# Kernel optimization log

Hardware: AMD Instinct MI355X
Metric: run time of the kernel (lower is better)

The kernel has to match this reference:

```python
import jax, jax.numpy as jnp
import numpy as np

D = 2048
H = 16
HD = 128
INNER = H * HD
EPS = 1e-6


def rmsnorm(x, w):
    var = jnp.mean(x * x, axis=-1, keepdims=True)
    return x * jax.lax.rsqrt(var + EPS) * w


def setup_inputs() -> dict:
    key = jax.random.key(0)
    ks = jax.random.split(key, 10)
    B, T, N_ws, T_corr = 2, 2048, 64, 512
    scale = 1.0 / np.sqrt(D)
    return {
        "hidden_states": jax.random.normal(ks[0], (B, T, D), jnp.float32),
        "workspace": jax.random.normal(ks[1], (B, N_ws, D), jnp.float32),
        "correction_tokens": jax.random.normal(ks[2], (B, T_corr, D), jnp.float32),
        "correction_mask": jax.random.randint(ks[3], (B, T_corr), 0, 2, jnp.int32),
        "ln_q_w": jnp.ones((D,), jnp.float32),
        "ln_kv_w": jnp.ones((D,), jnp.float32),
        "Wq": jax.random.normal(ks[4], (D, INNER), jnp.float32) * scale,
        "Wk": jax.random.normal(ks[5], (D, INNER), jnp.float32) * scale,
        "Wv": jax.random.normal(ks[6], (D, INNER), jnp.float32) * scale,
        "Wo": jax.random.normal(ks[7], (INNER, D), jnp.float32) * scale,
    }


def reference(hidden_states, workspace, correction_tokens, correction_mask,
              ln_q_w, ln_kv_w, Wq, Wk, Wv, Wo):
    B, T, _ = hidden_states.shape
    N_ws = workspace.shape[1]
    # kv context = [workspace ; correction_tokens]
    kv_context = jnp.concatenate([workspace, correction_tokens], axis=1)  # (B, N_kv, D)
    N_kv = kv_context.shape[1]
    ws_mask = jnp.ones((B, N_ws), hidden_states.dtype)
    kv_mask = jnp.concatenate([ws_mask, correction_mask.astype(hidden_states.dtype)], axis=1)  # (B, N_kv)

    h = rmsnorm(hidden_states, ln_q_w)
    kv = rmsnorm(kv_context, ln_kv_w)

    q = (h @ Wq).reshape(B, T, H, HD)        # (B,T,H,hd)
    k = (kv @ Wk).reshape(B, N_kv, H, HD)
    v = (kv @ Wv).reshape(B, N_kv, H, HD)

    scores = jnp.einsum("bthd,bshd->bhts", q, k) / np.sqrt(HD)  # (B,H,T,N_kv)
    mask = (kv_mask != 0)[:, None, None, :]                      # (B,1,1,N_kv)
    scores = jnp.where(mask, scores, -jnp.inf)
    attn = jax.nn.softmax(scores, axis=-1)
    attn = jnp.nan_to_num(attn, nan=0.0)
    # dropout is identity in eval mode
    out = jnp.einsum("bhts,bshd->bthd", attn, v).reshape(B, T, INNER)
    return out @ Wo
```

## Files before the change

### kernel.cpp

```cpp
#include <hip/hip_runtime.h>
#include <hip/hip_bf16.h>
#include <math.h>

typedef __bf16 bf16;
typedef __attribute__((ext_vector_type(8))) __bf16 bf16x8;
typedef __attribute__((ext_vector_type(4))) __bf16 bf16x4;
typedef __attribute__((ext_vector_type(4))) float f32x4;

#define D_DIM 2048
#define NKV   576

__device__ inline void gld_lds16(const void* g, void* l) {
    void* gg = const_cast<void*>(g);
    __builtin_amdgcn_global_load_lds(
        (__attribute__((address_space(1))) void*)gg,
        (__attribute__((address_space(3))) void*)l, 16, 0, 0);
}

#define PH_BARRIER() do { __builtin_amdgcn_s_barrier(); asm volatile("" ::: "memory"); } while (0)
#define VMCNT(n)     asm volatile("s_waitcnt vmcnt(" #n ")" ::: "memory")

__global__ __launch_bounds__(256) void prep(
    const float* __restrict__ hidden, const float* __restrict__ wsp,
    const float* __restrict__ corr, const float* __restrict__ lnq,
    const float* __restrict__ lnkv,
    const float* __restrict__ Wq, const float* __restrict__ Wk,
    const float* __restrict__ Wv, const float* __restrict__ Wo,
    bf16* __restrict__ hb, bf16* __restrict__ kvb,
    bf16* __restrict__ WqT, bf16* __restrict__ WkvT, bf16* __restrict__ WoT)
{
    __shared__ float tile[32][33];
    __shared__ float p[4];
    const int id = blockIdx.x, t = threadIdx.x;

    if (id < 16384) {
        const int wz = id >> 12, wy = (id >> 6) & 63, wx = id & 63;
        const float* in; bf16* out;
        switch (wz) {
            case 0:  in = Wq; out = WqT; break;
            case 1:  in = Wk; out = WkvT; break;
            case 2:  in = Wv; out = WkvT + 2048ull * 2048; break;
            default: in = Wo; out = WoT; break;
        }
        const int r0 = wy * 32, c0 = wx * 32;
        const int r = t >> 3, c = (t & 7) * 4;
        float4 v = *(const float4*)(in + (long)(r0 + r) * 2048 + c0 + c);
        tile[r][c] = v.x; tile[r][c + 1] = v.y;
        tile[r][c + 2] = v.z; tile[r][c + 3] = v.w;
        __syncthreads();
        bf16x4 o = { (bf16)tile[c][r], (bf16)tile[c + 1][r],
                     (bf16)tile[c + 2][r], (bf16)tile[c + 3][r] };
        *(bf16x4*)(out + (long)(c0 + r) * 2048 + r0 + c) = o;
        return;
    }

    const int rr0 = id - 16384;
    const float* xr; const float* w; bf16* yr;
    if (rr0 < 4096) {
        xr = hidden + (long)rr0 * D_DIM; w = lnq; yr = hb + (long)rr0 * D_DIM;
    } else if (rr0 < 4224) {
        const int rr = rr0 - 4096;
        xr = wsp + (long)rr * D_DIM; w = lnkv;
        yr = kvb + ((long)(rr >> 6) * NKV + (rr & 63)) * D_DIM;
    } else {
        const int rr = rr0 - 4224;
        xr = corr + (long)rr * D_DIM; w = lnkv;
        yr = kvb + ((long)(rr >> 9) * NKV + 64 + (rr & 511)) * D_DIM;
    }

    float4 v0 = *(const float4*)(xr + t * 4);
    float4 v1 = *(const float4*)(xr + 1024 + t * 4);
    float ss = v0.x * v0.x + v0.y * v0.y + v0.z * v0.z + v0.w * v0.w
             + v1.x * v1.x + v1.y * v1.y + v1.z * v1.z + v1.w * v1.w;
#pragma unroll
    for (int off = 32; off; off >>= 1) ss += __shfl_xor(ss, off);
    if ((t & 63) == 0) p[t >> 6] = ss;
    __syncthreads();
    const float rs = rsqrtf((p[0] + p[1] + p[2] + p[3]) * (1.0f / 2048.0f) + 1e-6f);

    float4 w0 = *(const float4*)(w + t * 4);
    float4 w1 = *(const float4*)(w + 1024 + t * 4);
    bf16x4 o0 = { (bf16)(v0.x * rs * w0.x), (bf16)(v0.y * rs * w0.y),
                  (bf16)(v0.z * rs * w0.z), (bf16)(v0.w * rs * w0.w) };
    bf16x4 o1 = { (bf16)(v1.x * rs * w1.x), (bf16)(v1.y * rs * w1.y),
                  (bf16)(v1.z * rs * w1.z), (bf16)(v1.w * rs * w1.w) };
    *(bf16x4*)(yr + t * 4) = o0;
    *(bf16x4*)(yr + 1024 + t * 4) = o1;
}

__global__ __launch_bounds__(512, 2) void proj_all(
    const bf16* __restrict__ hb, const bf16* __restrict__ kvb,
    const bf16* __restrict__ WqT, const bf16* __restrict__ WkvT,
    bf16* __restrict__ qb, bf16* __restrict__ kb, bf16* __restrict__ vtb)
{
    __shared__ __align__(16) bf16 smem[4][16384];
    bf16* const EA = smem[0]; bf16* const EB = smem[1];
    bf16* const OA = smem[2]; bf16* const OB = smem[3];

    const int id0 = blockIdx.x;
    const int id = (id0 & 7) * 26 + (id0 >> 3);
    const bf16 *A, *B; int m0, n0; bool isQ;
    if (id < 128) {
        isQ = true;  A = hb;  B = WqT;
        m0 = (id >> 3) * 256; n0 = (id & 7) * 256;
    } else {
        const int kd = id - 128;
        isQ = false; A = kvb; B = WkvT;
        m0 = (kd >> 4) * 256; n0 = (kd & 15) * 256;
    }

    const int tid = threadIdx.x, lane = tid & 63, w = tid >> 6;
    const int wm = (w >> 2) * 128, wn = (w & 3) * 64;
    const int fr = lane & 15, fg = lane >> 4;

    f32x4 acc[8][4] = {};
    bf16x8 af[4][2], bg[4][2];

    auto stage = [&](const bf16* base, int row0, int k, bf16* dst) {
#pragma unroll
        for (int q = 0; q < 2; ++q) {
            const int c = q * 512 + tid;
            const int r = c >> 3, cl = (c & 7) ^ (r & 7);
            gld_lds16(base + (long)(row0 + r) * 2048 + k + cl * 8, dst + c * 8);
        }
    };
    auto load_af = [&](const bf16* t, int ib) {
#pragma unroll
        for (int i = 0; i < 4; ++i)
#pragma unroll
            for (int s = 0; s < 2; ++s) {
                const int row = wm + (ib + i) * 16 + fr;
                af[i][s] = *(const bf16x8*)(t + ((row << 3) + ((s * 4 + fg) ^ (fr & 7))) * 8);
            }
    };
    auto load_bg = [&](const bf16* t, int jb) {
#pragma unroll
        for (int j = 0; j < 2; ++j)
#pragma unroll
            for (int s = 0; s < 2; ++s) {
                const int row = wn + (jb + j) * 16 + fr;
                bg[jb + j][s] = *(const bf16x8*)(t + ((row << 3) + ((s * 4 + fg) ^ (fr & 7))) * 8);
            }
    };
    auto mfma16 = [&](int ib, int jb) {
        __builtin_amdgcn_s_setprio(1);
#pragma unroll
        for (int s = 0; s < 2; ++s)
#pragma unroll
            for (int i = 0; i < 4; ++i)
#pragma unroll
                for (int j = 0; j < 2; ++j)
                    acc[ib + i][jb + j] = __builtin_amdgcn_mfma_f32_16x16x32_bf16(
                        af[i][s], bg[jb + j][s], acc[ib + i][jb + j], 0, 0, 0);
        __builtin_amdgcn_s_setprio(0);
    };

    stage(A, m0,        0, EA); stage(A, m0 + 128,  0, EA + 8192);
    stage(B, n0,        0, EB); stage(B, n0 + 128,  0, EB + 8192);
    stage(B, n0,       64, OB); stage(B, n0 + 128, 64, OB + 8192);
    VMCNT(4);
    PH_BARRIER();

    for (int it = 0; it < 16; ++it) {
        const int kO  = (it * 128 +  64) & 2047;
        const int kE2 = (it * 128 + 128) & 2047;
        const int kO2 = (it * 128 + 192) & 2047;
        load_af(EA, 0); load_bg(EB, 0);
        stage(A, m0, kO, OA);
        PH_BARRIER(); mfma16(0, 0); PH_BARRIER();
        load_bg(EB, 2);
        stage(A, m0 + 128, kO, OA + 8192);
        PH_BARRIER(); mfma16(0, 2); PH_BARRIER();
        load_af(EA, 4);
        stage(B, n0, kE2, EB);
        PH_BARRIER(); mfma16(4, 2); PH_BARRIER();
        stage(B, n0 + 128, kE2, EB + 8192);
        PH_BARRIER(); mfma16(4, 0); VMCNT(4); PH_BARRIER();
        load_af(OA, 0); load_bg(OB, 0);
        stage(A, m0, kE2, EA);
        PH_BARRIER(); mfma16(0, 0); PH_BARRIER();
        load_bg(OB, 2);
        stage(A, m0 + 128, kE2, EA + 8192);
        PH_BARRIER(); mfma16(0, 2); PH_BARRIER();
        load_af(OA, 4);
        stage(B, n0, kO2, OB);
        PH_BARRIER(); mfma16(4, 2); PH_BARRIER();
        stage(B, n0 + 128, kO2, OB + 8192);
        PH_BARRIER(); mfma16(4, 0); VMCNT(4); PH_BARRIER();
    }

    VMCNT(0);
    __syncthreads();

    const int er = fg * 4;
    if (isQ || n0 < 2048) {
        bf16* C = isQ ? qb : kb;
        const int mlim = isQ ? 4096 : 1152;
#pragma unroll
        for (int i = 0; i < 8; ++i)
#pragma unroll
            for (int j = 0; j < 4; ++j) {
                const int n = n0 + wn + j * 16 + fr;
#pragma unroll
                for (int r = 0; r < 4; ++r) {
                    const int m = m0 + wm + i * 16 + er + r;
                    if (m < mlim)
                        C[(long)m * 2048 + n] = (bf16)acc[i][j][r];
                }
            }
        return;
    }

    bf16* T = &smem[0][0];
#pragma unroll
    for (int p = 0; p < 2; ++p) {
        if (p) __syncthreads();
        if ((wn >> 7) == p) {
            const int nb = wn - p * 128;
#pragma unroll
            for (int i = 0; i < 8; ++i)
#pragma unroll
                for (int j = 0; j < 4; ++j) {
                    const int nl = nb + j * 16 + fr;
#pragma unroll
                    for (int r = 0; r < 4; ++r)
                        T[nl * 264 + wm + i * 16 + er + r] = (bf16)acc[i][j][r];
                }
        }
        __syncthreads();
        const int hh = (n0 - 2048 + p * 128) >> 7;
        for (int e = tid; e < 128 * 64; e += 512) {
            const int d = e >> 6, mg = (e & 63) * 4;
            const int mm = m0 + mg;
            if (mm < 1152) {
                bf16x4 val = *(const bf16x4*)(T + d * 264 + mg);
                const int bb = mm >= NKV;
                const int s = mm - bb * NKV;
                *(bf16x4*)(vtb + ((long)((bb * 16 + hh) * 128 + d)) * NKV + s) = val;
            }
        }
    }
}

__global__ __launch_bounds__(512, 2) void gemm_final(
    const bf16* __restrict__ Ag, const bf16* __restrict__ Bg, float* __restrict__ C)
{
    __shared__ __align__(16) bf16 smem[49152];
    bf16* const EA = smem;           bf16* const EB = smem + 16384;
    bf16* const OA = smem + 24576;   bf16* const OB = smem + 40960;

    const int id0 = blockIdx.x;
    const int id = (id0 & 7) * 32 + (id0 >> 3);
    const int m0 = (id >> 4) * 256, n0 = (id & 15) * 128;

    const int tid = threadIdx.x, lane = tid & 63, w = tid >> 6;
    const int wm = (w >> 1) * 64, wn = (w & 1) * 64;
    const int fr = lane & 15, fg = lane >> 4;

    f32x4 acc[4][4] = {};
    bf16x8 af[2][2], bg[4][2];

    auto stage = [&](const bf16* base, int row0, int k, bf16* dst) {
#pragma unroll
        for (int q = 0; q < 2; ++q) {
            const int c = q * 512 + tid;
            const int r = c >> 3, cl = (c & 7) ^ (r & 7);
            gld_lds16(base + (long)(row0 + r) * 2048 + k + cl * 8, dst + c * 8);
        }
    };
    auto load_af = [&](const bf16* t, int ib) {
#pragma unroll
        for (int i = 0; i < 2; ++i)
#pragma unroll
            for (int s = 0; s < 2; ++s) {
                const int row = wm + (ib + i) * 16 + fr;
                af[i][s] = *(const bf16x8*)(t + ((row << 3) + ((s * 4 + fg) ^ (fr & 7))) * 8);
            }
    };
    auto load_bg = [&](const bf16* t, int jb) {
#pragma unroll
        for (int j = 0; j < 2; ++j)
#pragma unroll
            for (int s = 0; s < 2; ++s) {
                const int row = wn + (jb + j) * 16 + fr;
                bg[jb + j][s] = *(const bf16x8*)(t + ((row << 3) + ((s * 4 + fg) ^ (fr & 7))) * 8);
            }
    };
    auto mfma8 = [&](int ib, int jb) {
        __builtin_amdgcn_s_setprio(1);
#pragma unroll
        for (int s = 0; s < 2; ++s)
#pragma unroll
            for (int i = 0; i < 2; ++i)
#pragma unroll
                for (int j = 0; j < 2; ++j)
                    acc[ib + i][jb + j] = __builtin_amdgcn_mfma_f32_16x16x32_bf16(
                        af[i][s], bg[jb + j][s], acc[ib + i][jb + j], 0, 0, 0);
        __builtin_amdgcn_s_setprio(0);
    };

    stage(Ag, m0,       0, EA); stage(Ag, m0 + 128, 0, EA + 8192);
    stage(Bg, n0,       0, EB);
    stage(Bg, n0,      64, OB);
    VMCNT(2);
    PH_BARRIER();

    for (int it = 0; it < 16; ++it) {
        const int kO  = (it * 128 +  64) & 2047;
        const int kE2 = (it * 128 + 128) & 2047;
        const int kO2 = (it * 128 + 192) & 2047;
        load_af(EA, 0); load_bg(EB, 0);
        stage(Ag, m0, kO, OA);
        PH_BARRIER(); mfma8(0, 0); PH_BARRIER();
        load_bg(EB, 2);
        stage(Ag, m0 + 128, kO, OA + 8192);
        PH_BARRIER(); mfma8(0, 2); PH_BARRIER();
        load_af(EA, 2);
        stage(Bg, n0, kE2, EB);
        PH_BARRIER(); mfma8(2, 2); PH_BARRIER();
        stage(Ag, m0, kE2, EA);
        PH_BARRIER(); mfma8(2, 0); VMCNT(4); PH_BARRIER();
        load_af(OA, 0); load_bg(OB, 0);
        stage(Ag, m0 + 128, kE2, EA + 8192);
        PH_BARRIER(); mfma8(0, 0); PH_BARRIER();
        load_bg(OB, 2);
        PH_BARRIER(); mfma8(0, 2); PH_BARRIER();
        load_af(OA, 2);
        stage(Bg, n0, kO2, OB);
        PH_BARRIER(); mfma8(2, 2); PH_BARRIER();
        PH_BARRIER(); mfma8(2, 0); VMCNT(2); PH_BARRIER();
    }

    VMCNT(0);
    __syncthreads();

    const int er = fg * 4;
#pragma unroll
    for (int i = 0; i < 4; ++i)
#pragma unroll
        for (int j = 0; j < 4; ++j) {
            const int n = n0 + wn + j * 16 + fr;
#pragma unroll
            for (int r = 0; r < 4; ++r)
                C[(long)(m0 + wm + i * 16 + er + r) * 2048 + n] = acc[i][j][r];
        }
}

__global__ __launch_bounds__(256, 4) void flash_attn(
    const bf16* __restrict__ Q, const bf16* __restrict__ K,
    const bf16* __restrict__ VT, const int* __restrict__ cmask,
    bf16* __restrict__ O)
{
    __shared__ __align__(16) bf16 Ks[64 * 128];
    __shared__ __align__(16) bf16 VTs[128 * 64];

    const int qt = blockIdx.x, h = blockIdx.y, b = blockIdx.z;
    const int tid = threadIdx.x, lane = tid & 63, w = tid >> 6;
    const int fr = lane & 15, fg = lane >> 4;

    const bf16* qbase = Q + ((long)(b * 2048 + qt * 64)) * 2048 + h * 128;
    bf16x8 qf[4];
#pragma unroll
    for (int s = 0; s < 4; ++s)
        qf[s] = *(const bf16x8*)(qbase + (long)(w * 16 + fr) * 2048 + s * 32 + fg * 8);

    float m_r[4], l_r[4];
    f32x4 acc_o[8];
#pragma unroll
    for (int r = 0; r < 4; ++r) { m_r[r] = -3.0e38f; l_r[r] = 0.f; }
#pragma unroll
    for (int j = 0; j < 8; ++j) acc_o[j] = (f32x4){0.f, 0.f, 0.f, 0.f};

    const float scale2 = 0.12752792330124195f;
    const bf16* kbase = K + (long)b * NKV * 2048 + h * 128;
    const bf16* vbase = VT + ((long)(b * 16 + h)) * 128 * NKV;

    for (int kc = 0; kc < 9; ++kc) {
        const int kv0 = kc * 64;
#pragma unroll
        for (int p = 0; p < 4; ++p) {
            const int c = p * 256 + tid;
            const int r = c >> 4, cs = c & 15, cl = cs ^ (r & 15);
            gld_lds16(kbase + (long)(kv0 + r) * 2048 + cl * 8, Ks + c * 8);
        }
#pragma unroll
        for (int p = 0; p < 4; ++p) {
            const int c = p * 256 + tid;
            const int r = c >> 3, cs = c & 7, cl = cs ^ (r & 7);
            gld_lds16(vbase + (long)r * NKV + kv0 + cl * 8, VTs + c * 8);
        }
        __syncthreads();

        f32x4 acc_s[4] = {};
#pragma unroll
        for (int s = 0; s < 4; ++s) {
#pragma unroll
            for (int j = 0; j < 4; ++j) {
                bf16x8 bg = *(const bf16x8*)(Ks +
                    ((j * 16 + fr) * 16 + ((s * 4 + fg) ^ fr)) * 8);
                acc_s[j] = __builtin_amdgcn_mfma_f32_16x16x32_bf16(qf[s], bg, acc_s[j], 0, 0, 0);
            }
        }

        float bias[4];
#pragma unroll
        for (int j = 0; j < 4; ++j) {
            const int kv = kv0 + j * 16 + fr;
            const bool valid = (kv < 64) || (cmask[b * 512 + kv - 64] != 0);
            bias[j] = valid ? 0.f : -1e30f;
        }
        float s_f[4][4];
        float mc[4] = {-3.0e38f, -3.0e38f, -3.0e38f, -3.0e38f};
#pragma unroll
        for (int j = 0; j < 4; ++j)
#pragma unroll
            for (int r = 0; r < 4; ++r) {
                float v = fmaf(acc_s[j][r], scale2, bias[j]);
                s_f[j][r] = v; mc[r] = fmaxf(mc[r], v);
            }
#pragma unroll
        for (int r = 0; r < 4; ++r) {
            mc[r] = fmaxf(mc[r], __shfl_xor(mc[r], 1));
            mc[r] = fmaxf(mc[r], __shfl_xor(mc[r], 2));
            mc[r] = fmaxf(mc[r], __shfl_xor(mc[r], 4));
            mc[r] = fmaxf(mc[r], __shfl_xor(mc[r], 8));
        }
        float alpha[4];
#pragma unroll
        for (int r = 0; r < 4; ++r) {
            const float mn = fmaxf(m_r[r], mc[r]);
            alpha[r] = __builtin_amdgcn_exp2f(m_r[r] - mn);
            m_r[r] = mn;
        }
        float rs[4] = {0.f, 0.f, 0.f, 0.f};
#pragma unroll
        for (int j = 0; j < 4; ++j)
#pragma unroll
            for (int r = 0; r < 4; ++r) {
                const float pv = __builtin_amdgcn_exp2f(s_f[j][r] - m_r[r]);
                s_f[j][r] = pv; rs[r] += pv;
            }
#pragma unroll
        for (int r = 0; r < 4; ++r) {
            rs[r] += __shfl_xor(rs[r], 1);
            rs[r] += __shfl_xor(rs[r], 2);
            rs[r] += __shfl_xor(rs[r], 4);
            rs[r] += __shfl_xor(rs[r], 8);
            l_r[r] = l_r[r] * alpha[r] + rs[r];
        }
#pragma unroll
        for (int j = 0; j < 8; ++j)
#pragma unroll
            for (int r = 0; r < 4; ++r) acc_o[j][r] *= alpha[r];

        __syncthreads();

        bf16* Ps = Ks;
#pragma unroll
        for (int j = 0; j < 4; ++j)
#pragma unroll
            for (int r = 0; r < 4; ++r)
                Ps[(w * 16 + fg * 4 + r) * 72 + j * 16 + fr] = (bf16)s_f[j][r];

#pragma unroll
        for (int s2 = 0; s2 < 2; ++s2) {
            bf16x8 af = *(const bf16x8*)(Ps + (w * 16 + fr) * 72 + s2 * 32 + fg * 8);
#pragma unroll
            for (int jd = 0; jd < 8; ++jd) {
                bf16x8 bg = *(const bf16x8*)(VTs +
                    ((jd * 16 + fr) * 8 + ((s2 * 4 + fg) ^ (fr & 7))) * 8);
                acc_o[jd] = __builtin_amdgcn_mfma_f32_16x16x32_bf16(af, bg, acc_o[jd], 0, 0, 0);
            }
        }
        __syncthreads();
    }

    bf16* obase = O + ((long)(b * 2048 + qt * 64)) * 2048 + h * 128;
#pragma unroll
    for (int r = 0; r < 4; ++r) {
        const float inv = 1.0f / l_r[r];
        const int row = w * 16 + fg * 4 + r;
#pragma unroll
        for (int jd = 0; jd < 8; ++jd)
            obase[(long)row * 2048 + jd * 16 + fr] = (bf16)(acc_o[jd][r] * inv);
    }
}

extern "C" void kernel_launch(void* const* d_in, const int* in_sizes, int n_in,
                              void* d_out, int out_size, void* d_ws, size_t ws_size,
                              hipStream_t stream)
{
    const float* hidden = (const float*)d_in[0];
    const float* wsp    = (const float*)d_in[1];
    const float* corr   = (const float*)d_in[2];
    const int*   cmask  = (const int*)d_in[3];
    const float* lnq    = (const float*)d_in[4];
    const float* lnkv   = (const float*)d_in[5];
    const float* Wq     = (const float*)d_in[6];
    const float* Wk     = (const float*)d_in[7];
    const float* Wv     = (const float*)d_in[8];
    const float* Wo     = (const float*)d_in[9];
    float* out = (float*)d_out;

    char* ws = (char*)d_ws;
    size_t off = 0;
    auto alloc = [&](size_t sz) { void* p = ws + off; off += (sz + 255) & ~(size_t)255; return p; };

    bf16* WqT   = (bf16*)alloc(2048ull * 2048 * 2);
    bf16* WkvT  = (bf16*)alloc(4096ull * 2048 * 2);
    bf16* WoT   = (bf16*)alloc(2048ull * 2048 * 2);
    bf16* hb    = (bf16*)alloc(4096ull * 2048 * 2);
    bf16* kvb   = (bf16*)alloc(1280ull * 2048 * 2);
    bf16* qb    = (bf16*)alloc(4096ull * 2048 * 2);
    bf16* kb    = (bf16*)alloc(1152ull * 2048 * 2);
    bf16* vtb   = (bf16*)alloc(4096ull * NKV * 2);
    bf16* aob   = (bf16*)alloc(4096ull * 2048 * 2);

    prep<<<21632, 256, 0, stream>>>(hidden, wsp, corr, lnq, lnkv,
                                    Wq, Wk, Wv, Wo, hb, kvb, WqT, WkvT, WoT);
    proj_all<<<208, 512, 0, stream>>>(hb, kvb, WqT, WkvT, qb, kb, vtb);
    flash_attn<<<dim3(32, 16, 2), 256, 0, stream>>>(qb, kb, vtb, cmask, aob);
    gemm_final<<<256, 512, 0, stream>>>(aob, WoT, out);
}
```

Measured before the change: 297.7 us.

## Enlarge weight-transpose tiles, precompute GEMM staging addresses, peel last K iteration

```diff
diff --git a/kernel.cpp b/kernel.cpp
--- a/kernel.cpp
+++ b/kernel.cpp
@@ -29,12 +29,13 @@
     bf16* __restrict__ hb, bf16* __restrict__ kvb,
     bf16* __restrict__ WqT, bf16* __restrict__ WkvT, bf16* __restrict__ WoT)
 {
-    __shared__ float tile[32][33];
+    __shared__ float tl[64][65];
     __shared__ float p[4];
     const int id = blockIdx.x, t = threadIdx.x;
 
-    if (id < 16384) {
-        const int wz = id >> 12, wy = (id >> 6) & 63, wx = id & 63;
+    if (id < 4096) {
+        const int wz = id >> 10, idx = id & 1023;
+        const int wy = idx >> 5, wx = idx & 31;
         const float* in; bf16* out;
         switch (wz) {
             case 0:  in = Wq; out = WqT; break;
@@ -42,19 +43,27 @@
             case 2:  in = Wv; out = WkvT + 2048ull * 2048; break;
             default: in = Wo; out = WoT; break;
         }
-        const int r0 = wy * 32, c0 = wx * 32;
-        const int r = t >> 3, c = (t & 7) * 4;
-        float4 v = *(const float4*)(in + (long)(r0 + r) * 2048 + c0 + c);
-        tile[r][c] = v.x; tile[r][c + 1] = v.y;
-        tile[r][c + 2] = v.z; tile[r][c + 3] = v.w;
+        const int r0 = wy * 64, c0 = wx * 64;
+        const int tr = t >> 4, tc = (t & 15) * 4;
+#pragma unroll
+        for (int q = 0; q < 4; ++q) {
+            const int r = tr + q * 16;
+            float4 v = *(const float4*)(in + (long)(r0 + r) * 2048 + c0 + tc);
+            tl[r][tc] = v.x; tl[r][tc + 1] = v.y;
+            tl[r][tc + 2] = v.z; tl[r][tc + 3] = v.w;
+        }
         __syncthreads();
-        bf16x4 o = { (bf16)tile[c][r], (bf16)tile[c + 1][r],
-                     (bf16)tile[c + 2][r], (bf16)tile[c + 3][r] };
-        *(bf16x4*)(out + (long)(c0 + r) * 2048 + r0 + c) = o;
+#pragma unroll
+        for (int q = 0; q < 4; ++q) {
+            const int orr = tr + q * 16;
+            bf16x4 o = { (bf16)tl[tc][orr], (bf16)tl[tc + 1][orr],
+                         (bf16)tl[tc + 2][orr], (bf16)tl[tc + 3][orr] };
+            *(bf16x4*)(out + (long)(c0 + orr) * 2048 + r0 + tc) = o;
+        }
         return;
     }
 
-    const int rr0 = id - 16384;
+    const int rr0 = id - 4096;
     const float* xr; const float* w; bf16* yr;
     if (rr0 < 4096) {
         xr = hidden + (long)rr0 * D_DIM; w = lnq; yr = hb + (long)rr0 * D_DIM;
@@ -116,31 +125,41 @@
     f32x4 acc[8][4] = {};
     bf16x8 af[4][2], bg[4][2];
 
-    auto stage = [&](const bf16* base, int row0, int k, bf16* dst) {
-#pragma unroll
-        for (int q = 0; q < 2; ++q) {
-            const int c = q * 512 + tid;
-            const int r = c >> 3, cl = (c & 7) ^ (r & 7);
-            gld_lds16(base + (long)(row0 + r) * 2048 + k + cl * 8, dst + c * 8);
-        }
-    };
-    auto load_af = [&](const bf16* t, int ib) {
+    const int aoff0 = (wm + fr) * 64 + (fg ^ (fr & 7)) * 8;
+    const int boff0 = (wn + fr) * 64 + (fg ^ (fr & 7)) * 8;
+    const int aoff1 = aoff0 ^ 32, boff1 = boff0 ^ 32;
+    const bf16* const pAE[2] = { EA + aoff0, EA + aoff1 };
+    const bf16* const pAO[2] = { OA + aoff0, OA + aoff1 };
+    const bf16* const pBE[2] = { EB + boff0, EB + boff1 };
+    const bf16* const pBO[2] = { OB + boff0, OB + boff1 };
+
+    const long toff = (long)(tid >> 3) * 2048 + (((tid & 7) ^ ((tid >> 3) & 7)) * 8);
+    const bf16* const gA0 = A + (long)m0 * 2048 + toff;
+    const bf16* const gA1 = gA0 + 262144;
+    const bf16* const gB0 = B + (long)n0 * 2048 + toff;
+    const bf16* const gB1 = gB0 + 262144;
+    bf16* const dT = (bf16*)smem + tid * 8;
+
+    auto stage2 = [&](const bf16* g, int k, int dslot) {
+        gld_lds16(g + k, dT + dslot);
+        gld_lds16(g + 131072 + k, dT + dslot + 4096);
+    };
+    enum { sEA0 = 0, sEA1 = 8192, sEB0 = 16384, sEB1 = 24576,
+           sOA0 = 32768, sOA1 = 40960, sOB0 = 49152, sOB1 = 57344 };
+
+    auto load_af = [&](const bf16* const p[2], int ib) {
 #pragma unroll
         for (int i = 0; i < 4; ++i)
 #pragma unroll
-            for (int s = 0; s < 2; ++s) {
-                const int row = wm + (ib + i) * 16 + fr;
-                af[i][s] = *(const bf16x8*)(t + ((row << 3) + ((s * 4 + fg) ^ (fr & 7))) * 8);
-            }
-    };
-    auto load_bg = [&](const bf16* t, int jb) {
+            for (int s = 0; s < 2; ++s)
+                af[i][s] = *(const bf16x8*)(p[s] + (ib + i) * 1024);
+    };
+    auto load_bg = [&](const bf16* const p[2], int jb) {
 #pragma unroll
         for (int j = 0; j < 2; ++j)
 #pragma unroll
-            for (int s = 0; s < 2; ++s) {
-                const int row = wn + (jb + j) * 16 + fr;
-                bg[jb + j][s] = *(const bf16x8*)(t + ((row << 3) + ((s * 4 + fg) ^ (fr & 7))) * 8);
-            }
+            for (int s = 0; s < 2; ++s)
+                bg[jb + j][s] = *(const bf16x8*)(p[s] + (jb + j) * 1024);
     };
     auto mfma16 = [&](int ib, int jb) {
         __builtin_amdgcn_s_setprio(1);
@@ -155,41 +174,56 @@
         __builtin_amdgcn_s_setprio(0);
     };
 
-    stage(A, m0,        0, EA); stage(A, m0 + 128,  0, EA + 8192);
-    stage(B, n0,        0, EB); stage(B, n0 + 128,  0, EB + 8192);
-    stage(B, n0,       64, OB); stage(B, n0 + 128, 64, OB + 8192);
+    stage2(gA0, 0, sEA0); stage2(gA1, 0, sEA1);
+    stage2(gB0, 0, sEB0); stage2(gB1, 0, sEB1);
+    stage2(gB0, 64, sOB0); stage2(gB1, 64, sOB1);
     VMCNT(4);
     PH_BARRIER();
 
-    for (int it = 0; it < 16; ++it) {
-        const int kO  = (it * 128 +  64) & 2047;
-        const int kE2 = (it * 128 + 128) & 2047;
-        const int kO2 = (it * 128 + 192) & 2047;
-        load_af(EA, 0); load_bg(EB, 0);
-        stage(A, m0, kO, OA);
+    for (int it = 0; it < 15; ++it) {
+        const int kO = it * 128 + 64, kE2 = it * 128 + 128, kO2 = it * 128 + 192;
+        load_af(pAE, 0); load_bg(pBE, 0);
+        stage2(gA0, kO, sOA0);
         PH_BARRIER(); mfma16(0, 0); PH_BARRIER();
-        load_bg(EB, 2);
-        stage(A, m0 + 128, kO, OA + 8192);
+        load_bg(pBE, 2);
+        stage2(gA1, kO, sOA1);
         PH_BARRIER(); mfma16(0, 2); PH_BARRIER();
-        load_af(EA, 4);
-        stage(B, n0, kE2, EB);
+        load_af(pAE, 4);
+        stage2(gB0, kE2, sEB0);
         PH_BARRIER(); mfma16(4, 2); PH_BARRIER();
-        stage(B, n0 + 128, kE2, EB + 8192);
+        stage2(gB1, kE2, sEB1);
         PH_BARRIER(); mfma16(4, 0); VMCNT(4); PH_BARRIER();
-        load_af(OA, 0); load_bg(OB, 0);
-        stage(A, m0, kE2, EA);
+        load_af(pAO, 0); load_bg(pBO, 0);
+        stage2(gA0, kE2, sEA0);
         PH_BARRIER(); mfma16(0, 0); PH_BARRIER();
-        load_bg(OB, 2);
-        stage(A, m0 + 128, kE2, EA + 8192);
+        load_bg(pBO, 2);
+        stage2(gA1, kE2, sEA1);
         PH_BARRIER(); mfma16(0, 2); PH_BARRIER();
-        load_af(OA, 4);
-        stage(B, n0, kO2, OB);
+        load_af(pAO, 4);
+        stage2(gB0, kO2, sOB0);
         PH_BARRIER(); mfma16(4, 2); PH_BARRIER();
-        stage(B, n0 + 128, kO2, OB + 8192);
+        stage2(gB1, kO2, sOB1);
         PH_BARRIER(); mfma16(4, 0); VMCNT(4); PH_BARRIER();
     }
-
-    VMCNT(0);
+    {
+        load_af(pAE, 0); load_bg(pBE, 0);
+        stage2(gA0, 1984, sOA0);
+        PH_BARRIER(); mfma16(0, 0); PH_BARRIER();
+        load_bg(pBE, 2);
+        stage2(gA1, 1984, sOA1);
+        PH_BARRIER(); mfma16(0, 2); PH_BARRIER();
+        load_af(pAE, 4);
+        PH_BARRIER(); mfma16(4, 2); PH_BARRIER();
+        PH_BARRIER(); mfma16(4, 0); VMCNT(0); PH_BARRIER();
+        load_af(pAO, 0); load_bg(pBO, 0);
+        PH_BARRIER(); mfma16(0, 0); PH_BARRIER();
+        load_bg(pBO, 2);
+        PH_BARRIER(); mfma16(0, 2); PH_BARRIER();
+        load_af(pAO, 4);
+        PH_BARRIER(); mfma16(4, 2); PH_BARRIER();
+        PH_BARRIER(); mfma16(4, 0); PH_BARRIER();
+    }
+
     __syncthreads();
 
     const int er = fg * 4;
@@ -213,10 +247,10 @@
 
     bf16* T = &smem[0][0];
 #pragma unroll
-    for (int p = 0; p < 2; ++p) {
-        if (p) __syncthreads();
-        if ((wn >> 7) == p) {
-            const int nb = wn - p * 128;
+    for (int p2 = 0; p2 < 2; ++p2) {
+        if (p2) __syncthreads();
+        if ((wn >> 7) == p2) {
+            const int nb = wn - p2 * 128;
 #pragma unroll
             for (int i = 0; i < 8; ++i)
 #pragma unroll
@@ -228,7 +262,7 @@
                 }
         }
         __syncthreads();
-        const int hh = (n0 - 2048 + p * 128) >> 7;
+        const int hh = (n0 - 2048 + p2 * 128) >> 7;
         for (int e = tid; e < 128 * 64; e += 512) {
             const int d = e >> 6, mg = (e & 63) * 4;
             const int mm = m0 + mg;
@@ -260,31 +294,40 @@
     f32x4 acc[4][4] = {};
     bf16x8 af[2][2], bg[4][2];
 
-    auto stage = [&](const bf16* base, int row0, int k, bf16* dst) {
-#pragma unroll
-        for (int q = 0; q < 2; ++q) {
-            const int c = q * 512 + tid;
-            const int r = c >> 3, cl = (c & 7) ^ (r & 7);
-            gld_lds16(base + (long)(row0 + r) * 2048 + k + cl * 8, dst + c * 8);
-        }
-    };
-    auto load_af = [&](const bf16* t, int ib) {
+    const int aoff0 = (wm + fr) * 64 + (fg ^ (fr & 7)) * 8;
+    const int boff0 = (wn + fr) * 64 + (fg ^ (fr & 7)) * 8;
+    const int aoff1 = aoff0 ^ 32, boff1 = boff0 ^ 32;
+    const bf16* const pAE[2] = { EA + aoff0, EA + aoff1 };
+    const bf16* const pAO[2] = { OA + aoff0, OA + aoff1 };
+    const bf16* const pBE[2] = { EB + boff0, EB + boff1 };
+    const bf16* const pBO[2] = { OB + boff0, OB + boff1 };
+
+    const long toff = (long)(tid >> 3) * 2048 + (((tid & 7) ^ ((tid >> 3) & 7)) * 8);
+    const bf16* const gA0 = Ag + (long)m0 * 2048 + toff;
+    const bf16* const gA1 = gA0 + 262144;
+    const bf16* const gB0 = Bg + (long)n0 * 2048 + toff;
+    bf16* const dT = smem + tid * 8;
+
+    auto stage2 = [&](const bf16* g, int k, int dslot) {
+        gld_lds16(g + k, dT + dslot);
+        gld_lds16(g + 131072 + k, dT + dslot + 4096);
+    };
+    enum { sEA0 = 0, sEA1 = 8192, sEB0 = 16384,
+           sOA0 = 24576, sOA1 = 32768, sOB0 = 40960 };
+
+    auto load_af = [&](const bf16* const p[2], int ib) {
 #pragma unroll
         for (int i = 0; i < 2; ++i)
 #pragma unroll
-            for (int s = 0; s < 2; ++s) {
-                const int row = wm + (ib + i) * 16 + fr;
-                af[i][s] = *(const bf16x8*)(t + ((row << 3) + ((s * 4 + fg) ^ (fr & 7))) * 8);
-            }
-    };
-    auto load_bg = [&](const bf16* t, int jb) {
+            for (int s = 0; s < 2; ++s)
+                af[i][s] = *(const bf16x8*)(p[s] + (ib + i) * 1024);
+    };
+    auto load_bg = [&](const bf16* const p[2], int jb) {
 #pragma unroll
         for (int j = 0; j < 2; ++j)
 #pragma unroll
-            for (int s = 0; s < 2; ++s) {
-                const int row = wn + (jb + j) * 16 + fr;
-                bg[jb + j][s] = *(const bf16x8*)(t + ((row << 3) + ((s * 4 + fg) ^ (fr & 7))) * 8);
-            }
+            for (int s = 0; s < 2; ++s)
+                bg[jb + j][s] = *(const bf16x8*)(p[s] + (jb + j) * 1024);
     };
     auto mfma8 = [&](int ib, int jb) {
         __builtin_amdgcn_s_setprio(1);
@@ -299,39 +342,54 @@
         __builtin_amdgcn_s_setprio(0);
     };
 
-    stage(Ag, m0,       0, EA); stage(Ag, m0 + 128, 0, EA + 8192);
-    stage(Bg, n0,       0, EB);
-    stage(Bg, n0,      64, OB);
+    stage2(gA0, 0, sEA0); stage2(gA1, 0, sEA1);
+    stage2(gB0, 0, sEB0);
+    stage2(gB0, 64, sOB0);
     VMCNT(2);
     PH_BARRIER();
 
-    for (int it = 0; it < 16; ++it) {
-        const int kO  = (it * 128 +  64) & 2047;
-        const int kE2 = (it * 128 + 128) & 2047;
-        const int kO2 = (it * 128 + 192) & 2047;
-        load_af(EA, 0); load_bg(EB, 0);
-        stage(Ag, m0, kO, OA);
+    for (int it = 0; it < 15; ++it) {
+        const int kO = it * 128 + 64, kE2 = it * 128 + 128, kO2 = it * 128 + 192;
+        load_af(pAE, 0); load_bg(pBE, 0);
+        stage2(gA0, kO, sOA0);
         PH_BARRIER(); mfma8(0, 0); PH_BARRIER();
-        load_bg(EB, 2);
-        stage(Ag, m0 + 128, kO, OA + 8192);
+        load_bg(pBE, 2);
+        stage2(gA1, kO, sOA1);
         PH_BARRIER(); mfma8(0, 2); PH_BARRIER();
-        load_af(EA, 2);
-        stage(Bg, n0, kE2, EB);
+        load_af(pAE, 2);
+        stage2(gB0, kE2, sEB0);
         PH_BARRIER(); mfma8(2, 2); PH_BARRIER();
-        stage(Ag, m0, kE2, EA);
+        stage2(gA0, kE2, sEA0);
         PH_BARRIER(); mfma8(2, 0); VMCNT(4); PH_BARRIER();
-        load_af(OA, 0); load_bg(OB, 0);
-        stage(Ag, m0 + 128, kE2, EA + 8192);
+        load_af(pAO, 0); load_bg(pBO, 0);
+        stage2(gA1, kE2, sEA1);
         PH_BARRIER(); mfma8(0, 0); PH_BARRIER();
-        load_bg(OB, 2);
+        load_bg(pBO, 2);
         PH_BARRIER(); mfma8(0, 2); PH_BARRIER();
-        load_af(OA, 2);
-        stage(Bg, n0, kO2, OB);
+        load_af(pAO, 2);
+        stage2(gB0, kO2, sOB0);
         PH_BARRIER(); mfma8(2, 2); PH_BARRIER();
         PH_BARRIER(); mfma8(2, 0); VMCNT(2); PH_BARRIER();
     }
-
-    VMCNT(0);
+    {
+        load_af(pAE, 0); load_bg(pBE, 0);
+        stage2(gA0, 1984, sOA0);
+        PH_BARRIER(); mfma8(0, 0); PH_BARRIER();
+        load_bg(pBE, 2);
+        stage2(gA1, 1984, sOA1);
+        PH_BARRIER(); mfma8(0, 2); PH_BARRIER();
+        load_af(pAE, 2);
+        PH_BARRIER(); mfma8(2, 2); PH_BARRIER();
+        PH_BARRIER(); mfma8(2, 0); VMCNT(0); PH_BARRIER();
+        load_af(pAO, 0); load_bg(pBO, 0);
+        PH_BARRIER(); mfma8(0, 0); PH_BARRIER();
+        load_bg(pBO, 2);
+        PH_BARRIER(); mfma8(0, 2); PH_BARRIER();
+        load_af(pAO, 2);
+        PH_BARRIER(); mfma8(2, 2); PH_BARRIER();
+        PH_BARRIER(); mfma8(2, 0); PH_BARRIER();
+    }
+
     __syncthreads();
 
     const int er = fg * 4;
@@ -396,9 +454,9 @@
         for (int s = 0; s < 4; ++s) {
 #pragma unroll
             for (int j = 0; j < 4; ++j) {
-                bf16x8 bg = *(const bf16x8*)(Ks +
+                bf16x8 bgv = *(const bf16x8*)(Ks +
                     ((j * 16 + fr) * 16 + ((s * 4 + fg) ^ fr)) * 8);
-                acc_s[j] = __builtin_amdgcn_mfma_f32_16x16x32_bf16(qf[s], bg, acc_s[j], 0, 0, 0);
+                acc_s[j] = __builtin_amdgcn_mfma_f32_16x16x32_bf16(qf[s], bgv, acc_s[j], 0, 0, 0);
             }
         }
 
@@ -464,12 +522,12 @@
 
 #pragma unroll
         for (int s2 = 0; s2 < 2; ++s2) {
-            bf16x8 af = *(const bf16x8*)(Ps + (w * 16 + fr) * 72 + s2 * 32 + fg * 8);
+            bf16x8 afv = *(const bf16x8*)(Ps + (w * 16 + fr) * 72 + s2 * 32 + fg * 8);
 #pragma unroll
             for (int jd = 0; jd < 8; ++jd) {
-                bf16x8 bg = *(const bf16x8*)(VTs +
+                bf16x8 bgv = *(const bf16x8*)(VTs +
                     ((jd * 16 + fr) * 8 + ((s2 * 4 + fg) ^ (fr & 7))) * 8);
-                acc_o[jd] = __builtin_amdgcn_mfma_f32_16x16x32_bf16(af, bg, acc_o[jd], 0, 0, 0);
+                acc_o[jd] = __builtin_amdgcn_mfma_f32_16x16x32_bf16(afv, bgv, acc_o[jd], 0, 0, 0);
             }
         }
         __syncthreads();
@@ -516,8 +574,8 @@
     bf16* vtb   = (bf16*)alloc(4096ull * NKV * 2);
     bf16* aob   = (bf16*)alloc(4096ull * 2048 * 2);
 
-    prep<<<21632, 256, 0, stream>>>(hidden, wsp, corr, lnq, lnkv,
-                                    Wq, Wk, Wv, Wo, hb, kvb, WqT, WkvT, WoT);
+    prep<<<9344, 256, 0, stream>>>(hidden, wsp, corr, lnq, lnkv,
+                                   Wq, Wk, Wv, Wo, hb, kvb, WqT, WkvT, WoT);
     proj_all<<<208, 512, 0, stream>>>(hb, kvb, WqT, WkvT, qb, kb, vtb);
     flash_attn<<<dim3(32, 16, 2), 256, 0, stream>>>(qb, kb, vtb, cmask, aob);
     gemm_final<<<256, 512, 0, stream>>>(aob, WoT, out);
```

Result: no change. 298.2 us (+0.1%).
